# Optimization experiments

Measured on AMD Instinct MI355X. Metric: run time of the kernel, lower is better.

The kernel has to match this reference:

```python
import jax, jax.numpy as jnp
import numpy as np

N, S, H, IN = 512, 128, 512, 2
INF = 1e7  # matches PointerNetAttention.inf


def setup_inputs() -> dict:
    key = jax.random.key(0)
    ks = jax.random.split(key, 12)
    u = lambda k, shp: jax.random.uniform(k, shp, jnp.float32, -0.08, 0.08)
    return {
        "x": jax.random.normal(ks[0], (N, S, IN), jnp.float32),
        "r": jax.random.normal(ks[1], (N, S, H), jnp.float32),
        "h0": jax.random.normal(ks[2], (1, N, H), jnp.float32) * 0.1,
        "c0": jax.random.normal(ks[3], (1, N, H), jnp.float32) * 0.1,
        # LSTM (num_layers=1), PyTorch layout: gates ordered i,f,g,o
        "W_ih": u(ks[4], (4 * H, IN)),
        "W_hh": u(ks[5], (4 * H, H)),
        "b_ih": u(ks[6], (4 * H,)),
        "b_hh": u(ks[7], (4 * H,)),
        # pointer attention params
        "w_ref": u(ks[8], (1, H, H)),
        "w_q": u(ks[9], (H, H)),
        "v": u(ks[10], (1, H)),
        "bos": u(ks[11], (1, 1, IN)),
    }


def reference(x, r, h0, c0, W_ih, W_hh, b_ih, b_hh, w_ref, w_q, v, bos):
    n, s, _ = r.shape
    # precompute encoder projection r @ w_ref once (loop-invariant)
    rW = jnp.einsum('nsh,hk->nsk', r, w_ref[0])
    init = (h0[0], c0[0],
            jnp.broadcast_to(bos[0, 0], (n, x.shape[2])),  # prev node = BOS
            jnp.zeros((n, s), r.dtype),                    # visited mask
            jnp.zeros((n,), r.dtype))                      # log-likelihood

    def step(carry, _):
        h, c, prev, mask, ll = carry
        # single-layer LSTM cell (seq len 1 per step)
        gates = prev @ W_ih.T + h @ W_hh.T + b_ih + b_hh
        i, f, g, o = jnp.split(gates, 4, axis=-1)
        c_new = jax.nn.sigmoid(f) * c + jax.nn.sigmoid(i) * jnp.tanh(g)
        h_new = jax.nn.sigmoid(o) * jnp.tanh(c_new)
        # pointer attention score
        q = h_new @ w_q
        score = jnp.einsum('nsh,h->ns', jnp.tanh(rW + q[:, None, :]), v[0]) - INF * mask
        logp = jax.nn.log_softmax(score, axis=1)
        pos = jnp.argmax(logp, axis=1)  # greedy selection
        ll = ll + jnp.take_along_axis(logp, pos[:, None], axis=1)[:, 0]
        mask = jnp.maximum(mask, jax.nn.one_hot(pos, s, dtype=mask.dtype))
        prev_new = jnp.take_along_axis(x, pos[:, None, None], axis=1)[:, 0, :]
        return (h_new, c_new, prev_new, mask, ll), pos

    (_, _, _, _, ll), tour = jax.lax.scan(step, init, None, length=s)
    return tour.T, ll  # pred_tour [N, S] (int), log_ll [N]
```

## Files before the change

### kernel.cpp

```cpp
#include <hip/hip_runtime.h>
#include <math.h>


namespace {
constexpr int NB  = 512;
constexpr int S   = 128;
constexpr int H   = 512;
constexpr int G   = 4;
constexpr int NBLK = NB / G;

__device__ __forceinline__ float ftanh(float x) {
  x = fminf(fmaxf(x, -15.f), 15.f);
  return 1.f - 2.f * __builtin_amdgcn_rcpf(__expf(2.f * x) + 1.f);
}
__device__ __forceinline__ float fsigm(float x) {
  x = fminf(fmaxf(x, -30.f), 30.f);
  return __builtin_amdgcn_rcpf(1.f + __expf(-x));
}

__device__ __forceinline__ void align_bar(int* bar, int target) {
  __syncthreads();
  if (threadIdx.x == 0) {
    __hip_atomic_fetch_add(bar, 1, __ATOMIC_RELAXED, __HIP_MEMORY_SCOPE_AGENT);
    int it = 0;
    while (__hip_atomic_load(bar, __ATOMIC_RELAXED, __HIP_MEMORY_SCOPE_AGENT) < target
           && ++it < (1 << 20))
      __builtin_amdgcn_s_sleep(2);
  }
  __syncthreads();
}
}

__global__ void k_zero(int* bar) { if (threadIdx.x == 0) *bar = 0; }

__global__ __launch_bounds__(256) void k_pack(const float* __restrict__ Whh,
                                              const float* __restrict__ wq,
                                              float* __restrict__ whhp,
                                              float* __restrict__ wqp) {
  int i = blockIdx.x * 256 + threadIdx.x;
  if (i < 2048 * 512) {
    int m = i >> 9, k = i & 511;
    whhp[(size_t)(k >> 2) * 8192 + m * 4 + (k & 3)] = Whh[i];
  }
  int j2 = i - 2048 * 512;
  if (j2 >= 0 && j2 < 512 * 512) {
    int k = j2 >> 9, j = j2 & 511;
    wqp[(size_t)(k >> 2) * 2048 + j * 4 + (k & 3)] = wq[j2];
  }
}

__global__ __launch_bounds__(256) void k_rw(const float* __restrict__ r,
                                            const float* __restrict__ wref,
                                            float* __restrict__ rW) {
  __shared__ float As[16][64];
  __shared__ float Bs[16][64];
  const int tid = threadIdx.x;
  const int tx = tid & 15, ty = tid >> 4;
  const int M0 = blockIdx.x * 64, N0 = blockIdx.y * 64;
  float acc[4][4] = {};
  for (int k0 = 0; k0 < H; k0 += 16) {
    {
      int row = tid >> 2, c4 = (tid & 3) * 4;
      float4 a = *(const float4*)&r[(size_t)(M0 + row) * H + k0 + c4];
      As[c4+0][row] = a.x; As[c4+1][row] = a.y; As[c4+2][row] = a.z; As[c4+3][row] = a.w;
    }
    {
      int row = tid >> 4, c4 = (tid & 15) * 4;
      *(float4*)&Bs[row][c4] = *(const float4*)&wref[(size_t)(k0 + row) * H + N0 + c4];
    }
    __syncthreads();
#pragma unroll
    for (int kk = 0; kk < 16; ++kk) {
      float4 a = *(float4*)&As[kk][ty*4];
      float4 b = *(float4*)&Bs[kk][tx*4];
      float av[4] = {a.x,a.y,a.z,a.w}, bv[4] = {b.x,b.y,b.z,b.w};
#pragma unroll
      for (int i = 0; i < 4; ++i)
#pragma unroll
        for (int j = 0; j < 4; ++j) acc[i][j] += av[i]*bv[j];
    }
    __syncthreads();
  }
#pragma unroll
  for (int i = 0; i < 4; ++i)
    *(float4*)&rW[(size_t)(M0 + ty*4 + i) * H + N0 + tx*4] =
        make_float4(acc[i][0], acc[i][1], acc[i][2], acc[i][3]);
}

struct DecArgs {
  const float *x, *h0, *c0, *Wih, *bih, *bhh, *v, *bos;
  const float *whhp, *wqp, *rW;
  float *out_tour, *out_ll;
  int *bar;
};

__global__ __launch_bounds__(512) void k_decode(DecArgs a) {
  const int tid  = threadIdx.x;
  const int b    = blockIdx.x;
  const int n0   = b * G;
  const int lane = tid & 63, wave = tid >> 6;

  __shared__ float h_[2][G][H];
  __shared__ float c_[G][H];
  __shared__ float q_[G][H];
  __shared__ float sc_[G][S];
  __shared__ unsigned short alive_[G][S];
  __shared__ unsigned short inv_[G][S];
  __shared__ int   cnt_[G];
  __shared__ float prev_[G][2];
  __shared__ float ll_[G];

  for (int i = tid; i < G * H; i += 512) {
    int n = i >> 9, k = i & 511;
    h_[0][n][k] = a.h0[(size_t)(n0 + n) * H + k];
    c_[n][k]    = a.c0[(size_t)(n0 + n) * H + k];
  }
  for (int i = tid; i < G * S; i += 512) {
    alive_[i >> 7][i & 127] = (unsigned short)(i & 127);
    inv_[i >> 7][i & 127]   = (unsigned short)(i & 127);
  }
  if (tid < G) {
    cnt_[tid] = S;
    ll_[tid] = 0.f;
    prev_[tid][0] = a.bos[0];
    prev_[tid][1] = a.bos[1];
  }

  float bsum[4], wi0[4], wi1[4];
#pragma unroll
  for (int g = 0; g < 4; ++g) {
    int m = g * H + tid;
    bsum[g] = a.bih[m] + a.bhh[m];
    wi0[g]  = a.Wih[2 * m];
    wi1[g]  = a.Wih[2 * m + 1];
  }
  const float4 vA = *(const float4*)&a.v[lane * 8];
  const float4 vB = *(const float4*)&a.v[lane * 8 + 4];
  __syncthreads();

  for (int t = 0; t < S; ++t) {
    align_bar(a.bar, (t + 1) * NBLK);

    const int cur = t & 1, nxt = cur ^ 1;

    {
      float acc[G][4] = {};
#pragma unroll 2
      for (int k4 = 0; k4 < 128; ++k4) {
        float4 h4[G];
#pragma unroll
        for (int n = 0; n < G; ++n) h4[n] = *(const float4*)&h_[cur][n][k4 * 4];
        const float* wp = &a.whhp[(size_t)k4 * 8192 + tid * 4];
#pragma unroll
        for (int g = 0; g < 4; ++g) {
          float4 w4 = *(const float4*)&wp[g * 2048];
#pragma unroll
          for (int n = 0; n < G; ++n)
            acc[n][g] += h4[n].x * w4.x + h4[n].y * w4.y
                       + h4[n].z * w4.z + h4[n].w * w4.w;
        }
      }
#pragma unroll
      for (int n = 0; n < G; ++n) {
        float p0 = prev_[n][0], p1 = prev_[n][1];
        float gv[4];
#pragma unroll
        for (int g = 0; g < 4; ++g)
          gv[g] = acc[n][g] + bsum[g] + p0 * wi0[g] + p1 * wi1[g];
        float cv = c_[n][tid];
        float cn = fsigm(gv[1]) * cv + fsigm(gv[0]) * ftanh(gv[2]);
        float hn = fsigm(gv[3]) * ftanh(cn);
        c_[n][tid] = cn;
        h_[nxt][n][tid] = hn;
      }
    }
    __syncthreads();

    {
      float accq[G] = {};
#pragma unroll 4
      for (int k4 = 0; k4 < 128; ++k4) {
        float4 w4 = *(const float4*)&a.wqp[(size_t)k4 * 2048 + tid * 4];
#pragma unroll
        for (int n = 0; n < G; ++n) {
          float4 h4 = *(const float4*)&h_[nxt][n][k4 * 4];
          accq[n] += h4.x * w4.x + h4.y * w4.y + h4.z * w4.z + h4.w * w4.w;
        }
      }
#pragma unroll
      for (int n = 0; n < G; ++n) q_[n][tid] = accq[n];
    }
    __syncthreads();

    {
      const int n    = wave >> 1;
      const int half = wave & 1;
      const int cnt  = cnt_[n];
      const float4 qA = *(const float4*)&q_[n][lane * 8];
      const float4 qB = *(const float4*)&q_[n][lane * 8 + 4];
      const float* rwn = a.rW + (size_t)(n0 + n) * S * H + lane * 8;
#pragma unroll 1
      for (int c0 = half * 8; c0 < cnt; c0 += 16) {
        int rows[8];
        float4 A0[8], A1[8];
#pragma unroll
        for (int rr = 0; rr < 8; ++rr) {
          int idx = c0 + rr; if (idx > cnt - 1) idx = cnt - 1;
          rows[rr] = alive_[n][idx];
        }
#pragma unroll
        for (int rr = 0; rr < 8; ++rr) {
          const float* rp = rwn + (size_t)rows[rr] * H;
          A0[rr] = *(const float4*)rp;
          A1[rr] = *(const float4*)(rp + 4);
        }
#pragma unroll
        for (int rr = 0; rr < 8; ++rr) {
          float sr = ftanh(A0[rr].x + qA.x) * vA.x + ftanh(A0[rr].y + qA.y) * vA.y
                   + ftanh(A0[rr].z + qA.z) * vA.z + ftanh(A0[rr].w + qA.w) * vA.w
                   + ftanh(A1[rr].x + qB.x) * vB.x + ftanh(A1[rr].y + qB.y) * vB.y
                   + ftanh(A1[rr].z + qB.z) * vB.z + ftanh(A1[rr].w + qB.w) * vB.w;
#pragma unroll
          for (int off = 32; off > 0; off >>= 1) sr += __shfl_down(sr, off);
          if (lane == 0) sc_[n][rows[rr]] = sr;
        }
      }
    }
    __syncthreads();

    if (wave < G) {
      const int n = wave;
      const int cnt = cnt_[n];
      float bv = -3.4e38f; int bi = 1 << 30;
      for (int i = lane; i < cnt; i += 64) {
        int s = alive_[n][i];
        float vv = sc_[n][s];
        if (vv > bv || (vv == bv && s < bi)) { bv = vv; bi = s; }
      }
#pragma unroll
      for (int off = 32; off > 0; off >>= 1) {
        float ov = __shfl_down(bv, off);
        int   oi = __shfl_down(bi, off);
        if (ov > bv || (ov == bv && oi < bi)) { bv = ov; bi = oi; }
      }
      bv = __shfl(bv, 0); bi = __shfl(bi, 0);
      float e = 0.f;
      for (int i = lane; i < cnt; i += 64) {
        int s = alive_[n][i];
        e += __expf(sc_[n][s] - bv);
      }
#pragma unroll
      for (int off = 32; off > 0; off >>= 1) e += __shfl_down(e, off);
      if (lane == 0) {
        float nll = ll_[n] - logf(e);
        ll_[n] = nll;
        a.out_ll[n0 + n] = nll;
        a.out_tour[(size_t)(n0 + n) * S + t] = (float)bi;
        int p = inv_[n][bi];
        unsigned short last = alive_[n][cnt - 1];
        alive_[n][p] = last;
        inv_[n][last] = (unsigned short)p;
        cnt_[n] = cnt - 1;
        prev_[n][0] = a.x[((size_t)(n0 + n) * S + bi) * 2 + 0];
        prev_[n][1] = a.x[((size_t)(n0 + n) * S + bi) * 2 + 1];
      }
    }
    __syncthreads();
  }
}

extern "C" void kernel_launch(void* const* d_in, const int* in_sizes, int n_in,
                              void* d_out, int out_size, void* d_ws, size_t ws_size,
                              hipStream_t stream) {
  const float* x    = (const float*)d_in[0];
  const float* r    = (const float*)d_in[1];
  const float* h0   = (const float*)d_in[2];
  const float* c0   = (const float*)d_in[3];
  const float* Wih  = (const float*)d_in[4];
  const float* Whh  = (const float*)d_in[5];
  const float* bih  = (const float*)d_in[6];
  const float* bhh  = (const float*)d_in[7];
  const float* wref = (const float*)d_in[8];
  const float* wq   = (const float*)d_in[9];
  const float* v    = (const float*)d_in[10];
  const float* bos  = (const float*)d_in[11];
  float* out = (float*)d_out;
  float* ws  = (float*)d_ws;

  size_t off = 0;
  float* rW   = ws + off; off += (size_t)NB * S * H;
  float* whhp = ws + off; off += (size_t)4 * H * H;
  float* wqp  = ws + off; off += (size_t)H * H;
  int*   bar  = (int*)(ws + off); off += 16;

  k_zero<<<1, 64, 0, stream>>>(bar);
  k_pack<<<(2048*512 + 512*512 + 255) / 256, 256, 0, stream>>>(Whh, wq, whhp, wqp);
  k_rw<<<dim3(NB * S / 64, H / 64), 256, 0, stream>>>(r, wref, rW);

  DecArgs da;
  da.x = x; da.h0 = h0; da.c0 = c0; da.Wih = Wih; da.bih = bih; da.bhh = bhh;
  da.v = v; da.bos = bos; da.whhp = whhp; da.wqp = wqp; da.rW = rW;
  da.out_tour = out; da.out_ll = out + (size_t)NB * S;
  da.bar = bar;

  k_decode<<<NBLK, 512, 0, stream>>>(da);
}
```

Measured before the change: 13.27 ms.

## Double decode block threads, split batch rows across halves, use nontemporal rW loads

The decode kernel now runs 1024 threads per block. Each half-block computes the LSTM gate GEMV and the q projection for two of the four batch rows, so every thread does half the FMA work, while the weight loads are duplicated across the halves. The attention scoring now uses four waves per row instead of two, and the rW loads become nontemporal to avoid polluting the cache. The goal is to shorten per-step latency inside the serial 128-step loop, at the cost of doubled weight-read traffic per block and higher register pressure under the new launch bounds.

```diff
diff --git a/kernel.cpp b/kernel.cpp
--- a/kernel.cpp
+++ b/kernel.cpp
@@ -9,6 +9,8 @@
 constexpr int G   = 4;
 constexpr int NBLK = NB / G;
 
+typedef float f32x4 __attribute__((ext_vector_type(4)));
+
 __device__ __forceinline__ float ftanh(float x) {
   x = fminf(fmaxf(x, -15.f), 15.f);
   return 1.f - 2.f * __builtin_amdgcn_rcpf(__expf(2.f * x) + 1.f);
@@ -16,6 +18,9 @@
 __device__ __forceinline__ float fsigm(float x) {
   x = fminf(fmaxf(x, -30.f), 30.f);
   return __builtin_amdgcn_rcpf(1.f + __expf(-x));
+}
+__device__ __forceinline__ float dot4(f32x4 h, f32x4 w) {
+  return h.x * w.x + h.y * w.y + h.z * w.z + h.w * w.w;
 }
 
 __device__ __forceinline__ void align_bar(int* bar, int target) {
@@ -94,11 +99,12 @@
   int *bar;
 };
 
-__global__ __launch_bounds__(512) void k_decode(DecArgs a) {
+__global__ __launch_bounds__(1024, 4) void k_decode(DecArgs a) {
   const int tid  = threadIdx.x;
   const int b    = blockIdx.x;
   const int n0   = b * G;
   const int lane = tid & 63, wave = tid >> 6;
+  const int j    = tid & 511, nh = tid >> 9;
 
   __shared__ float h_[2][G][H];
   __shared__ float c_[G][H];
@@ -110,12 +116,12 @@
   __shared__ float prev_[G][2];
   __shared__ float ll_[G];
 
-  for (int i = tid; i < G * H; i += 512) {
+  for (int i = tid; i < G * H; i += 1024) {
     int n = i >> 9, k = i & 511;
     h_[0][n][k] = a.h0[(size_t)(n0 + n) * H + k];
     c_[n][k]    = a.c0[(size_t)(n0 + n) * H + k];
   }
-  for (int i = tid; i < G * S; i += 512) {
+  for (int i = tid; i < G * S; i += 1024) {
     alive_[i >> 7][i & 127] = (unsigned short)(i & 127);
     inv_[i >> 7][i & 127]   = (unsigned short)(i & 127);
   }
@@ -129,80 +135,96 @@
   float bsum[4], wi0[4], wi1[4];
 #pragma unroll
   for (int g = 0; g < 4; ++g) {
-    int m = g * H + tid;
+    int m = g * H + j;
     bsum[g] = a.bih[m] + a.bhh[m];
     wi0[g]  = a.Wih[2 * m];
     wi1[g]  = a.Wih[2 * m + 1];
   }
-  const float4 vA = *(const float4*)&a.v[lane * 8];
-  const float4 vB = *(const float4*)&a.v[lane * 8 + 4];
+  const f32x4 vA = *(const f32x4*)&a.v[lane * 8];
+  const f32x4 vB = *(const f32x4*)&a.v[lane * 8 + 4];
   __syncthreads();
 
   for (int t = 0; t < S; ++t) {
     align_bar(a.bar, (t + 1) * NBLK);
-
     const int cur = t & 1, nxt = cur ^ 1;
 
     {
-      float acc[G][4] = {};
-#pragma unroll 2
-      for (int k4 = 0; k4 < 128; ++k4) {
-        float4 h4[G];
-#pragma unroll
-        for (int n = 0; n < G; ++n) h4[n] = *(const float4*)&h_[cur][n][k4 * 4];
-        const float* wp = &a.whhp[(size_t)k4 * 8192 + tid * 4];
-#pragma unroll
-        for (int g = 0; g < 4; ++g) {
-          float4 w4 = *(const float4*)&wp[g * 2048];
-#pragma unroll
-          for (int n = 0; n < G; ++n)
-            acc[n][g] += h4[n].x * w4.x + h4[n].y * w4.y
-                       + h4[n].z * w4.z + h4[n].w * w4.w;
-        }
-      }
-#pragma unroll
-      for (int n = 0; n < G; ++n) {
+      float acc[2][4] = {};
+      const float* hp0 = &h_[cur][nh * 2 + 0][0];
+      const float* hp1 = &h_[cur][nh * 2 + 1][0];
+#pragma unroll 1
+      for (int k8 = 0; k8 < 64; ++k8) {
+        const float* wpa = a.whhp + (size_t)k8 * 16384 + j * 4;
+        f32x4 wa0 = *(const f32x4*)(wpa + 0);
+        f32x4 wa1 = *(const f32x4*)(wpa + 2048);
+        f32x4 wa2 = *(const f32x4*)(wpa + 4096);
+        f32x4 wa3 = *(const f32x4*)(wpa + 6144);
+        f32x4 wb0 = *(const f32x4*)(wpa + 8192);
+        f32x4 wb1 = *(const f32x4*)(wpa + 10240);
+        f32x4 wb2 = *(const f32x4*)(wpa + 12288);
+        f32x4 wb3 = *(const f32x4*)(wpa + 14336);
+        f32x4 h0a = *(const f32x4*)&hp0[k8 * 8];
+        f32x4 h0b = *(const f32x4*)&hp0[k8 * 8 + 4];
+        f32x4 h1a = *(const f32x4*)&hp1[k8 * 8];
+        f32x4 h1b = *(const f32x4*)&hp1[k8 * 8 + 4];
+        acc[0][0] += dot4(h0a, wa0) + dot4(h0b, wb0);
+        acc[0][1] += dot4(h0a, wa1) + dot4(h0b, wb1);
+        acc[0][2] += dot4(h0a, wa2) + dot4(h0b, wb2);
+        acc[0][3] += dot4(h0a, wa3) + dot4(h0b, wb3);
+        acc[1][0] += dot4(h1a, wa0) + dot4(h1b, wb0);
+        acc[1][1] += dot4(h1a, wa1) + dot4(h1b, wb1);
+        acc[1][2] += dot4(h1a, wa2) + dot4(h1b, wb2);
+        acc[1][3] += dot4(h1a, wa3) + dot4(h1b, wb3);
+      }
+#pragma unroll
+      for (int i = 0; i < 2; ++i) {
+        int n = nh * 2 + i;
         float p0 = prev_[n][0], p1 = prev_[n][1];
         float gv[4];
 #pragma unroll
         for (int g = 0; g < 4; ++g)
-          gv[g] = acc[n][g] + bsum[g] + p0 * wi0[g] + p1 * wi1[g];
-        float cv = c_[n][tid];
+          gv[g] = acc[i][g] + bsum[g] + p0 * wi0[g] + p1 * wi1[g];
+        float cv = c_[n][j];
         float cn = fsigm(gv[1]) * cv + fsigm(gv[0]) * ftanh(gv[2]);
         float hn = fsigm(gv[3]) * ftanh(cn);
-        c_[n][tid] = cn;
-        h_[nxt][n][tid] = hn;
-      }
-    }
-    __syncthreads();
-
-    {
-      float accq[G] = {};
-#pragma unroll 4
-      for (int k4 = 0; k4 < 128; ++k4) {
-        float4 w4 = *(const float4*)&a.wqp[(size_t)k4 * 2048 + tid * 4];
-#pragma unroll
-        for (int n = 0; n < G; ++n) {
-          float4 h4 = *(const float4*)&h_[nxt][n][k4 * 4];
-          accq[n] += h4.x * w4.x + h4.y * w4.y + h4.z * w4.z + h4.w * w4.w;
-        }
-      }
-#pragma unroll
-      for (int n = 0; n < G; ++n) q_[n][tid] = accq[n];
-    }
-    __syncthreads();
-
-    {
-      const int n    = wave >> 1;
-      const int half = wave & 1;
-      const int cnt  = cnt_[n];
-      const float4 qA = *(const float4*)&q_[n][lane * 8];
-      const float4 qB = *(const float4*)&q_[n][lane * 8 + 4];
+        c_[n][j] = cn;
+        h_[nxt][n][j] = hn;
+      }
+    }
+    __syncthreads();
+
+    {
+      float accq[2] = {};
+      const float* hp0 = &h_[nxt][nh * 2 + 0][0];
+      const float* hp1 = &h_[nxt][nh * 2 + 1][0];
+#pragma unroll 1
+      for (int k8 = 0; k8 < 64; ++k8) {
+        const float* wp = a.wqp + (size_t)k8 * 4096 + j * 4;
+        f32x4 w0 = *(const f32x4*)(wp + 0);
+        f32x4 w1 = *(const f32x4*)(wp + 2048);
+        f32x4 h0a = *(const f32x4*)&hp0[k8 * 8];
+        f32x4 h0b = *(const f32x4*)&hp0[k8 * 8 + 4];
+        f32x4 h1a = *(const f32x4*)&hp1[k8 * 8];
+        f32x4 h1b = *(const f32x4*)&hp1[k8 * 8 + 4];
+        accq[0] += dot4(h0a, w0) + dot4(h0b, w1);
+        accq[1] += dot4(h1a, w0) + dot4(h1b, w1);
+      }
+      q_[nh * 2 + 0][j] = accq[0];
+      q_[nh * 2 + 1][j] = accq[1];
+    }
+    __syncthreads();
+
+    {
+      const int n  = wave >> 2;
+      const int qr = wave & 3;
+      const int cnt = cnt_[n];
+      const f32x4 qA = *(const f32x4*)&q_[n][lane * 8];
+      const f32x4 qB = *(const f32x4*)&q_[n][lane * 8 + 4];
       const float* rwn = a.rW + (size_t)(n0 + n) * S * H + lane * 8;
 #pragma unroll 1
-      for (int c0 = half * 8; c0 < cnt; c0 += 16) {
+      for (int c0 = qr * 8; c0 < cnt; c0 += 32) {
         int rows[8];
-        float4 A0[8], A1[8];
+        f32x4 A0[8], A1[8];
 #pragma unroll
         for (int rr = 0; rr < 8; ++rr) {
           int idx = c0 + rr; if (idx > cnt - 1) idx = cnt - 1;
@@ -211,15 +233,15 @@
 #pragma unroll
         for (int rr = 0; rr < 8; ++rr) {
           const float* rp = rwn + (size_t)rows[rr] * H;
-          A0[rr] = *(const float4*)rp;
-          A1[rr] = *(const float4*)(rp + 4);
+          A0[rr] = __builtin_nontemporal_load((const f32x4*)rp);
+          A1[rr] = __builtin_nontemporal_load((const f32x4*)(rp + 4));
         }
 #pragma unroll
         for (int rr = 0; rr < 8; ++rr) {
-          float sr = ftanh(A0[rr].x + qA.x) * vA.x + ftanh(A0[rr].y + qA.y) * vA.y
-                   + ftanh(A0[rr].z + qA.z) * vA.z + ftanh(A0[rr].w + qA.w) * vA.w
-                   + ftanh(A1[rr].x + qB.x) * vB.x + ftanh(A1[rr].y + qB.y) * vB.y
-                   + ftanh(A1[rr].z + qB.z) * vB.z + ftanh(A1[rr].w + qB.w) * vB.w;
+          float sr = ftanh(A0[rr].x + qA.x)*vA.x + ftanh(A0[rr].y + qA.y)*vA.y
+                   + ftanh(A0[rr].z + qA.z)*vA.z + ftanh(A0[rr].w + qA.w)*vA.w
+                   + ftanh(A1[rr].x + qB.x)*vB.x + ftanh(A1[rr].y + qB.y)*vB.y
+                   + ftanh(A1[rr].z + qB.z)*vB.z + ftanh(A1[rr].w + qB.w)*vB.w;
 #pragma unroll
           for (int off = 32; off > 0; off >>= 1) sr += __shfl_down(sr, off);
           if (lane == 0) sc_[n][rows[rr]] = sr;
@@ -245,10 +267,7 @@
       }
       bv = __shfl(bv, 0); bi = __shfl(bi, 0);
       float e = 0.f;
-      for (int i = lane; i < cnt; i += 64) {
-        int s = alive_[n][i];
-        e += __expf(sc_[n][s] - bv);
-      }
+      for (int i = lane; i < cnt; i += 64) e += __expf(sc_[n][alive_[n][i]] - bv);
 #pragma unroll
       for (int off = 32; off > 0; off >>= 1) e += __shfl_down(e, off);
       if (lane == 0) {
@@ -303,5 +322,5 @@
   da.out_tour = out; da.out_ll = out + (size_t)NB * S;
   da.bar = bar;
 
-  k_decode<<<NBLK, 512, 0, stream>>>(da);
-}
+  k_decode<<<NBLK, 1024, 0, stream>>>(da);
+}
```

Result: slower. 15.78 ms (+18.9%).
